# Optimization experiments

Hardware: AMD Instinct MI355X
Metric: run time of the kernel (lower is better)

Reference implementation:

```python
import jax, jax.numpy as jnp
import numpy as np

NUM_SLOTS = 24
EPS = 1e-5

def setup_inputs() -> dict:
    key = jax.random.key(0)
    k1, k2 = jax.random.split(key)
    x = jax.random.normal(k1, (4, 32, 200, 2048), dtype=jnp.float32)
    time = jax.random.randint(k2, (4, 2048), 0, NUM_SLOTS, dtype=jnp.int64)
    return {"x": x, "time": time}

def reference(x, time):
    # x: [b, c, n, t]; time: [b, t] int slot ids in [0, NUM_SLOTS)
    b, c, n, t = x.shape
    time = time[..., -t:]
    idx = time.reshape(b * t)

    # [b*t, n, c] layout matching x.permute(2,0,3,1).reshape(n, b*t, c) contraction
    xf = jnp.transpose(x, (0, 3, 2, 1)).reshape(b * t, n * c)

    # True segment-sum replaces the one-hot matmul; column L1-normalize == divide by slot count
    counts = jax.ops.segment_sum(jnp.ones((b * t,), x.dtype), idx, num_segments=NUM_SLOTS)
    denom = jnp.maximum(counts, 1e-12)[:, None]  # F.normalize eps-clamped norm

    sum_x = jax.ops.segment_sum(xf, idx, num_segments=NUM_SLOTS)            # [S, n*c]
    sum_x2 = jax.ops.segment_sum(xf * xf, idx, num_segments=NUM_SLOTS)      # [S, n*c]

    mean_slot = (sum_x / denom).reshape(NUM_SLOTS, n, c).mean(axis=1)       # [S, c]
    m2_slot = (sum_x2 / denom).reshape(NUM_SLOTS, n, c).mean(axis=1)        # [S, c]
    var_slot = m2_slot - mean_slot ** 2                                     # [S, c]

    # Embedding gather back per (b, t), broadcast over n
    sm = jnp.transpose(mean_slot[time], (0, 2, 1))[:, :, None, :]           # [b, c, 1, t]
    sv = jnp.transpose(var_slot[time], (0, 2, 1))[:, :, None, :]            # [b, c, 1, t]

    return (x - sm) / jnp.sqrt(sv + EPS)
```

## Files before the change

kernel.cpp:

```cpp
#include <hip/hip_runtime.h>
#include <math.h>

#define Bb 4
#define Cc 32
#define Nn 200
#define Tt 2048
#define Ss 24
#define EPSf 1e-5f
#define GRID2 512

typedef float f4 __attribute__((ext_vector_type(4)));
typedef int i4 __attribute__((ext_vector_type(4)));
typedef unsigned u4 __attribute__((ext_vector_type(4)));

__device__ __forceinline__ unsigned rne_bf16(float f) {
    unsigned u = __float_as_uint(f);
    return (u + 0x7FFFu + ((u >> 16) & 1u)) >> 16;
}
__device__ __forceinline__ unsigned pack2(float a, float b) {
    return rne_bf16(a) | (rne_bf16(b) << 16);
}
__device__ __forceinline__ float lo16(unsigned u) { return __uint_as_float(u << 16); }
__device__ __forceinline__ float hi16(unsigned u) { return __uint_as_float(u & 0xFFFF0000u); }


__global__ void k_zero(int* __restrict__ counter) { *counter = 0; }

#define ROWS16(M) M(0) M(1) M(2) M(3) M(4) M(5) M(6) M(7) \
                  M(8) M(9) M(10) M(11) M(12) M(13) M(14) M(15)

#define DROW(i) u4 xb##i;

#define LROW(i) { \
    f4 v0 = *(const f4*)(bp + (size_t)(i) * Tt); \
    f4 v1 = *(const f4*)(bp + (size_t)(i) * Tt + 4); \
    xb##i[0] = pack2(v0[0], v0[1]); \
    xb##i[1] = pack2(v0[2], v0[3]); \
    xb##i[2] = pack2(v1[0], v1[1]); \
    xb##i[3] = pack2(v1[2], v1[3]); \
    s0 += v0[0]; a0 += v0[0]*v0[0]; s1 += v0[1]; a1 += v0[1]*v0[1]; \
    s2 += v0[2]; a2 += v0[2]*v0[2]; s3 += v0[3]; a3 += v0[3]*v0[3]; \
    s4 += v1[0]; a4 += v1[0]*v1[0]; s5 += v1[1]; a5 += v1[1]*v1[1]; \
    s6 += v1[2]; a6 += v1[2]*v1[2]; s7 += v1[3]; a7 += v1[3]*v1[3]; }

#define SROW(i) { \
    f4 o0, o1; \
    o0[0] = fmaf(lo16(xb##i[0]), rr0, -mr0); \
    o0[1] = fmaf(hi16(xb##i[0]), rr1, -mr1); \
    o0[2] = fmaf(lo16(xb##i[1]), rr2, -mr2); \
    o0[3] = fmaf(hi16(xb##i[1]), rr3, -mr3); \
    o1[0] = fmaf(lo16(xb##i[2]), rr4, -mr4); \
    o1[1] = fmaf(hi16(xb##i[2]), rr5, -mr5); \
    o1[2] = fmaf(lo16(xb##i[3]), rr6, -mr6); \
    o1[3] = fmaf(hi16(xb##i[3]), rr7, -mr7); \
    __builtin_nontemporal_store(o0, (f4*)(op + (size_t)(i) * Tt)); \
    __builtin_nontemporal_store(o1, (f4*)(op + (size_t)(i) * Tt + 4)); }

__global__ __launch_bounds__(512) void k_fused(const float* __restrict__ x,
                                               const int* __restrict__ timei,
                                               float2* __restrict__ part,
                                               int* __restrict__ cntp,
                                               int* __restrict__ counter,
                                               float* __restrict__ out) {
    __shared__ unsigned ldsd[9 * 4 * 512];
    __shared__ float lsum[Ss], lsq[Ss];
    __shared__ int   lcnt[Ss];
    __shared__ float s_r[Ss], s_mr[Ss];

    const int tid = threadIdx.x;
    const int bx  = blockIdx.x;
    const int b   = bx >> 7;
    const int c   = (bx >> 2) & 31;
    const int qc  = bx & 3;
    const int rg  = tid >> 8;
    const int t0  = (tid & 255) * 8;

    if (tid < Ss) { lsum[tid] = 0.f; lsq[tid] = 0.f; lcnt[tid] = 0; }
    __syncthreads();

    const i4 sl0 = *(const i4*)(timei + b * Tt + t0);
    const i4 sl1 = *(const i4*)(timei + b * Tt + t0 + 4);

    const size_t plane = ((size_t)(b * Cc + c) * Nn + (size_t)qc * 50 + (size_t)rg * 25) * Tt + t0;
    const float* bp = x + plane;

    ROWS16(DROW)
    float s0=0,s1=0,s2=0,s3=0,s4=0,s5=0,s6=0,s7=0;
    float a0=0,a1=0,a2=0,a3=0,a4=0,a5=0,a6=0,a7=0;

    ROWS16(LROW)
    for (int r = 16; r < 25; ++r) {
        f4 v0 = *(const f4*)(bp + (size_t)r * Tt);
        f4 v1 = *(const f4*)(bp + (size_t)r * Tt + 4);
        const int base = (r - 16) * 4 * 512 + tid;
        ldsd[base]        = pack2(v0[0], v0[1]);
        ldsd[base + 512]  = pack2(v0[2], v0[3]);
        ldsd[base + 1024] = pack2(v1[0], v1[1]);
        ldsd[base + 1536] = pack2(v1[2], v1[3]);
        s0 += v0[0]; a0 += v0[0]*v0[0]; s1 += v0[1]; a1 += v0[1]*v0[1];
        s2 += v0[2]; a2 += v0[2]*v0[2]; s3 += v0[3]; a3 += v0[3]*v0[3];
        s4 += v1[0]; a4 += v1[0]*v1[0]; s5 += v1[1]; a5 += v1[1]*v1[1];
        s6 += v1[2]; a6 += v1[2]*v1[2]; s7 += v1[3]; a7 += v1[3]*v1[3];
    }

    atomicAdd(&lsum[sl0[0]], s0); atomicAdd(&lsq[sl0[0]], a0);
    atomicAdd(&lsum[sl0[1]], s1); atomicAdd(&lsq[sl0[1]], a1);
    atomicAdd(&lsum[sl0[2]], s2); atomicAdd(&lsq[sl0[2]], a2);
    atomicAdd(&lsum[sl0[3]], s3); atomicAdd(&lsq[sl0[3]], a3);
    atomicAdd(&lsum[sl1[0]], s4); atomicAdd(&lsq[sl1[0]], a4);
    atomicAdd(&lsum[sl1[1]], s5); atomicAdd(&lsq[sl1[1]], a5);
    atomicAdd(&lsum[sl1[2]], s6); atomicAdd(&lsq[sl1[2]], a6);
    atomicAdd(&lsum[sl1[3]], s7); atomicAdd(&lsq[sl1[3]], a7);
    if (c == 0 && qc == 0 && rg == 0) {
        atomicAdd(&lcnt[sl0[0]], 1); atomicAdd(&lcnt[sl0[1]], 1);
        atomicAdd(&lcnt[sl0[2]], 1); atomicAdd(&lcnt[sl0[3]], 1);
        atomicAdd(&lcnt[sl1[0]], 1); atomicAdd(&lcnt[sl1[1]], 1);
        atomicAdd(&lcnt[sl1[2]], 1); atomicAdd(&lcnt[sl1[3]], 1);
    }
    __syncthreads();

    if (tid < Ss) {
        part[(c * Ss + tid) * 16 + (b * 4 + qc)] = make_float2(lsum[tid], lsq[tid]);
        if (c == 0 && qc == 0) cntp[b * Ss + tid] = lcnt[tid];
    }
    __syncthreads();

    if (tid == 0) {
        __threadfence();
        __hip_atomic_fetch_add(counter, 1, __ATOMIC_ACQ_REL, __HIP_MEMORY_SCOPE_AGENT);
        while (__hip_atomic_load(counter, __ATOMIC_ACQUIRE, __HIP_MEMORY_SCOPE_AGENT) < GRID2)
            __builtin_amdgcn_s_sleep(2);
        __threadfence();
    }
    __syncthreads();

    if (tid < Ss) { lsum[tid] = 0.f; lsq[tid] = 0.f; }
    __syncthreads();
    if (tid < 192) {
        const int s = tid >> 3, j = tid & 7;
        float2 p0 = part[(c * Ss + s) * 16 + 2 * j];
        float2 p1 = part[(c * Ss + s) * 16 + 2 * j + 1];
        atomicAdd(&lsum[s], p0.x + p1.x);
        atomicAdd(&lsq[s],  p0.y + p1.y);
    }
    __syncthreads();
    if (tid < Ss) {
        int cnt = cntp[tid] + cntp[Ss + tid] + cntp[2 * Ss + tid] + cntp[3 * Ss + tid];
        float denom = fmaxf((float)cnt, 1e-12f) * (float)Nn;
        float m  = lsum[tid] / denom;
        float m2 = lsq[tid]  / denom;
        float rr = 1.0f / sqrtf(m2 - m * m + EPSf);
        s_r[tid]  = rr;
        s_mr[tid] = m * rr;
    }
    __syncthreads();

    const float rr0 = s_r[sl0[0]], mr0 = s_mr[sl0[0]];
    const float rr1 = s_r[sl0[1]], mr1 = s_mr[sl0[1]];
    const float rr2 = s_r[sl0[2]], mr2 = s_mr[sl0[2]];
    const float rr3 = s_r[sl0[3]], mr3 = s_mr[sl0[3]];
    const float rr4 = s_r[sl1[0]], mr4 = s_mr[sl1[0]];
    const float rr5 = s_r[sl1[1]], mr5 = s_mr[sl1[1]];
    const float rr6 = s_r[sl1[2]], mr6 = s_mr[sl1[2]];
    const float rr7 = s_r[sl1[3]], mr7 = s_mr[sl1[3]];

    float* op = out + plane;
    ROWS16(SROW)
    for (int r = 16; r < 25; ++r) {
        const int base = (r - 16) * 4 * 512 + tid;
        const unsigned w0 = ldsd[base];
        const unsigned w1 = ldsd[base + 512];
        const unsigned w2 = ldsd[base + 1024];
        const unsigned w3 = ldsd[base + 1536];
        f4 o0, o1;
        o0[0] = fmaf(lo16(w0), rr0, -mr0);
        o0[1] = fmaf(hi16(w0), rr1, -mr1);
        o0[2] = fmaf(lo16(w1), rr2, -mr2);
        o0[3] = fmaf(hi16(w1), rr3, -mr3);
        o1[0] = fmaf(lo16(w2), rr4, -mr4);
        o1[1] = fmaf(hi16(w2), rr5, -mr5);
        o1[2] = fmaf(lo16(w3), rr6, -mr6);
        o1[3] = fmaf(hi16(w3), rr7, -mr7);
        __builtin_nontemporal_store(o0, (f4*)(op + (size_t)r * Tt));
        __builtin_nontemporal_store(o1, (f4*)(op + (size_t)r * Tt + 4));
    }
}

__global__ __launch_bounds__(256) void k_stats(const float* __restrict__ x,
                                               const int* __restrict__ timei,
                                               float2* __restrict__ part,
                                               int* __restrict__ cntpart) {
    __shared__ float lsum[Ss], lsq[Ss];
    __shared__ int   lcnt[Ss];
    const int tid = threadIdx.x;
    const int bx  = blockIdx.x;
    const int tt = bx & 1;
    const int nc = (bx >> 1) & 7;
    const int bc = bx >> 4;
    const int b  = bc >> 5;
    const int c  = bc & 31;
    const bool do_hist = (c == 0 && nc == 0);

    if (tid < Ss) { lsum[tid] = 0.f; lsq[tid] = 0.f; lcnt[tid] = 0; }
    __syncthreads();

    const int t0 = tt * 1024 + tid * 4;
    const i4 sl = *(const i4*)(timei + b * Tt + t0);

    const size_t plane = ((size_t)(b * Cc + c) * Nn + (size_t)nc * 25) * Tt;
    const float* bp = x + plane + t0;

    float s0 = 0.f, s1 = 0.f, s2 = 0.f, s3 = 0.f;
    float q0 = 0.f, q1 = 0.f, q2 = 0.f, q3 = 0.f;
#pragma unroll 5
    for (int r = 0; r < 25; ++r) {
        f4 v = *(const f4*)(bp + (size_t)r * Tt);
        s0 += v[0]; q0 += v[0] * v[0];
        s1 += v[1]; q1 += v[1] * v[1];
        s2 += v[2]; q2 += v[2] * v[2];
        s3 += v[3]; q3 += v[3] * v[3];
    }

    atomicAdd(&lsum[sl[0]], s0); atomicAdd(&lsq[sl[0]], q0);
    atomicAdd(&lsum[sl[1]], s1); atomicAdd(&lsq[sl[1]], q1);
    atomicAdd(&lsum[sl[2]], s2); atomicAdd(&lsq[sl[2]], q2);
    atomicAdd(&lsum[sl[3]], s3); atomicAdd(&lsq[sl[3]], q3);
    if (do_hist) {
        atomicAdd(&lcnt[sl[0]], 1); atomicAdd(&lcnt[sl[1]], 1);
        atomicAdd(&lcnt[sl[2]], 1); atomicAdd(&lcnt[sl[3]], 1);
    }
    __syncthreads();

    const int chunk = (b * 2 + tt) * 8 + nc;
    if (tid < Ss) {
        part[(c * Ss + tid) * 64 + chunk] = make_float2(lsum[tid], lsq[tid]);
        if (do_hist) cntpart[(b * 2 + tt) * Ss + tid] = lcnt[tid];
    }
}

__global__ __launch_bounds__(256) void k_norm(const float* __restrict__ x,
                                              const int* __restrict__ timei,
                                              const float2* __restrict__ part,
                                              const int* __restrict__ cntpart,
                                              float* __restrict__ out) {
    __shared__ float lsum[Ss], lsq[Ss];
    __shared__ float s_mr[Ss], s_r[Ss];
    const int tid = threadIdx.x;
    const int bx  = blockIdx.x;
    const int b  = bx >> 7;
    const int c  = (bx >> 2) & 31;
    const int nc = bx & 3;

    if (tid < Ss) { lsum[tid] = 0.f; lsq[tid] = 0.f; }
    __syncthreads();
    if (tid < 192) {
        const int s = tid >> 3, j = tid & 7;
        const float2* pp = &part[(c * Ss + s) * 64 + j * 8];
        float ps = 0.f, pq = 0.f;
#pragma unroll
        for (int k = 0; k < 8; ++k) { ps += pp[k].x; pq += pp[k].y; }
        atomicAdd(&lsum[s], ps);
        atomicAdd(&lsq[s],  pq);
    }
    __syncthreads();
    if (tid < Ss) {
        int cnt = 0;
#pragma unroll
        for (int h = 0; h < 8; ++h) cnt += cntpart[h * Ss + tid];
        float denom = fmaxf((float)cnt, 1e-12f) * (float)Nn;
        float m  = lsum[tid] / denom;
        float m2 = lsq[tid]  / denom;
        float rr = 1.0f / sqrtf(m2 - m * m + EPSf);
        s_r[tid]  = rr;
        s_mr[tid] = m * rr;
    }
    __syncthreads();

    const int t0 = tid * 4;
    const i4 sl0 = *(const i4*)(timei + b * Tt + t0);
    const i4 sl1 = *(const i4*)(timei + b * Tt + t0 + 1024);
    const float rr0 = s_r[sl0[0]], mr0 = s_mr[sl0[0]];
    const float rr1 = s_r[sl0[1]], mr1 = s_mr[sl0[1]];
    const float rr2 = s_r[sl0[2]], mr2 = s_mr[sl0[2]];
    const float rr3 = s_r[sl0[3]], mr3 = s_mr[sl0[3]];
    const float rr4 = s_r[sl1[0]], mr4 = s_mr[sl1[0]];
    const float rr5 = s_r[sl1[1]], mr5 = s_mr[sl1[1]];
    const float rr6 = s_r[sl1[2]], mr6 = s_mr[sl1[2]];
    const float rr7 = s_r[sl1[3]], mr7 = s_mr[sl1[3]];

    const size_t plane = ((size_t)(b * Cc + c) * Nn + (size_t)nc * 50) * Tt;
    const float* xp = x + plane + t0;
    float* op = out + plane + t0;

#pragma unroll 5
    for (int r = 0; r < 50; ++r) {
        f4 v0 = *(const f4*)(xp + (size_t)r * Tt);
        f4 v1 = *(const f4*)(xp + (size_t)r * Tt + 1024);
        f4 o0, o1;
        o0[0] = fmaf(v0[0], rr0, -mr0);
        o0[1] = fmaf(v0[1], rr1, -mr1);
        o0[2] = fmaf(v0[2], rr2, -mr2);
        o0[3] = fmaf(v0[3], rr3, -mr3);
        o1[0] = fmaf(v1[0], rr4, -mr4);
        o1[1] = fmaf(v1[1], rr5, -mr5);
        o1[2] = fmaf(v1[2], rr6, -mr6);
        o1[3] = fmaf(v1[3], rr7, -mr7);
        __builtin_nontemporal_store(o0, (f4*)(op + (size_t)r * Tt));
        __builtin_nontemporal_store(o1, (f4*)(op + (size_t)r * Tt + 1024));
    }
}

extern "C" void kernel_launch(void* const* d_in, const int* in_sizes, int n_in,
                              void* d_out, int out_size, void* d_ws, size_t ws_size,
                              hipStream_t stream) {
    const float* x   = (const float*)d_in[0];
    const int* timei = (const int*)d_in[1];
    float* out = (float*)d_out;

    hipFuncAttributes fa;
    bool fused_ok = (hipFuncGetAttributes(&fa, (const void*)k_fused) == hipSuccess)
                    && fa.localSizeBytes == 0;
    if (fused_ok) {
        int occ = 0;
        fused_ok = (hipOccupancyMaxActiveBlocksPerMultiprocessor(&occ, k_fused, 512, 0)
                    == hipSuccess) && occ >= 2;
    }

    if (fused_ok) {
        float2* part = (float2*)d_ws;
        int* cntp    = (int*)((char*)d_ws + (size_t)Cc * Ss * 64 * sizeof(float2));
        int* counter = (int*)((char*)d_ws + (size_t)Cc * Ss * 64 * sizeof(float2)
                              + 128 * sizeof(int));
        k_zero<<<1, 1, 0, stream>>>(counter);
        k_fused<<<GRID2, 512, 0, stream>>>(x, timei, part, cntp, counter, out);
    } else {
        float2* part = (float2*)d_ws;
        int* cnt = (int*)((char*)d_ws + (size_t)Cc * Ss * 64 * sizeof(float2));
        k_stats<<<2048, 256, 0, stream>>>(x, timei, part, cnt);
        k_norm<<<512, 256, 0, stream>>>(x, timei, part, cnt, out);
    }
}
```

Measured before the change: 104.0 us.

## Split fused kernel caching: fewer register rows, smaller LDS, re-read tail rows

```diff
diff --git a/kernel.cpp b/kernel.cpp
--- a/kernel.cpp
+++ b/kernel.cpp
@@ -7,7 +7,7 @@
 #define Tt 2048
 #define Ss 24
 #define EPSf 1e-5f
-#define GRID2 512
+#define GRIDF 512
 
 typedef float f4 __attribute__((ext_vector_type(4)));
 typedef int i4 __attribute__((ext_vector_type(4)));
@@ -26,14 +26,13 @@
 
 __global__ void k_zero(int* __restrict__ counter) { *counter = 0; }
 
-#define ROWS16(M) M(0) M(1) M(2) M(3) M(4) M(5) M(6) M(7) \
-                  M(8) M(9) M(10) M(11) M(12) M(13) M(14) M(15)
+#define ROWS12(M) M(0) M(1) M(2) M(3) M(4) M(5) M(6) M(7) M(8) M(9) M(10) M(11)
 
 #define DROW(i) u4 xb##i;
 
 #define LROW(i) { \
     f4 v0 = *(const f4*)(bp + (size_t)(i) * Tt); \
-    f4 v1 = *(const f4*)(bp + (size_t)(i) * Tt + 4); \
+    f4 v1 = *(const f4*)(bp + (size_t)(i) * Tt + 1024); \
     xb##i[0] = pack2(v0[0], v0[1]); \
     xb##i[1] = pack2(v0[2], v0[3]); \
     xb##i[2] = pack2(v1[0], v1[1]); \
@@ -54,45 +53,46 @@
     o1[2] = fmaf(lo16(xb##i[3]), rr6, -mr6); \
     o1[3] = fmaf(hi16(xb##i[3]), rr7, -mr7); \
     __builtin_nontemporal_store(o0, (f4*)(op + (size_t)(i) * Tt)); \
-    __builtin_nontemporal_store(o1, (f4*)(op + (size_t)(i) * Tt + 4)); }
-
-__global__ __launch_bounds__(512) void k_fused(const float* __restrict__ x,
+    __builtin_nontemporal_store(o1, (f4*)(op + (size_t)(i) * Tt + 1024)); }
+
+__global__ __launch_bounds__(512) void k_fuse2(const float* __restrict__ x,
                                                const int* __restrict__ timei,
                                                float2* __restrict__ part,
                                                int* __restrict__ cntp,
                                                int* __restrict__ counter,
                                                float* __restrict__ out) {
-    __shared__ unsigned ldsd[9 * 4 * 512];
+    __shared__ unsigned ldsd[7 * 4 * 512];
     __shared__ float lsum[Ss], lsq[Ss];
     __shared__ int   lcnt[Ss];
     __shared__ float s_r[Ss], s_mr[Ss];
 
-    const int tid = threadIdx.x;
-    const int bx  = blockIdx.x;
-    const int b   = bx >> 7;
-    const int c   = (bx >> 2) & 31;
-    const int qc  = bx & 3;
-    const int rg  = tid >> 8;
-    const int t0  = (tid & 255) * 8;
+    const int tid  = threadIdx.x;
+    const int bx   = blockIdx.x;
+    const int b    = bx >> 7;
+    const int c    = (bx >> 2) & 31;
+    const int q    = bx & 3;
+    const int rg   = tid >> 8;
+    const int lane = tid & 255;
+    const int t0   = lane * 4;
 
     if (tid < Ss) { lsum[tid] = 0.f; lsq[tid] = 0.f; lcnt[tid] = 0; }
     __syncthreads();
 
     const i4 sl0 = *(const i4*)(timei + b * Tt + t0);
-    const i4 sl1 = *(const i4*)(timei + b * Tt + t0 + 4);
-
-    const size_t plane = ((size_t)(b * Cc + c) * Nn + (size_t)qc * 50 + (size_t)rg * 25) * Tt + t0;
+    const i4 sl1 = *(const i4*)(timei + b * Tt + t0 + 1024);
+
+    const size_t plane = ((size_t)(b * Cc + c) * Nn + (size_t)q * 50 + (size_t)rg * 25) * Tt + t0;
     const float* bp = x + plane;
 
-    ROWS16(DROW)
+    ROWS12(DROW)
     float s0=0,s1=0,s2=0,s3=0,s4=0,s5=0,s6=0,s7=0;
     float a0=0,a1=0,a2=0,a3=0,a4=0,a5=0,a6=0,a7=0;
 
-    ROWS16(LROW)
-    for (int r = 16; r < 25; ++r) {
+    ROWS12(LROW)
+    for (int r = 12; r < 19; ++r) {
         f4 v0 = *(const f4*)(bp + (size_t)r * Tt);
-        f4 v1 = *(const f4*)(bp + (size_t)r * Tt + 4);
-        const int base = (r - 16) * 4 * 512 + tid;
+        f4 v1 = *(const f4*)(bp + (size_t)r * Tt + 1024);
+        const int base = (r - 12) * 2048 + tid;
         ldsd[base]        = pack2(v0[0], v0[1]);
         ldsd[base + 512]  = pack2(v0[2], v0[3]);
         ldsd[base + 1024] = pack2(v1[0], v1[1]);
@@ -102,6 +102,14 @@
         s4 += v1[0]; a4 += v1[0]*v1[0]; s5 += v1[1]; a5 += v1[1]*v1[1];
         s6 += v1[2]; a6 += v1[2]*v1[2]; s7 += v1[3]; a7 += v1[3]*v1[3];
     }
+    for (int r = 19; r < 25; ++r) {
+        f4 v0 = *(const f4*)(bp + (size_t)r * Tt);
+        f4 v1 = *(const f4*)(bp + (size_t)r * Tt + 1024);
+        s0 += v0[0]; a0 += v0[0]*v0[0]; s1 += v0[1]; a1 += v0[1]*v0[1];
+        s2 += v0[2]; a2 += v0[2]*v0[2]; s3 += v0[3]; a3 += v0[3]*v0[3];
+        s4 += v1[0]; a4 += v1[0]*v1[0]; s5 += v1[1]; a5 += v1[1]*v1[1];
+        s6 += v1[2]; a6 += v1[2]*v1[2]; s7 += v1[3]; a7 += v1[3]*v1[3];
+    }
 
     atomicAdd(&lsum[sl0[0]], s0); atomicAdd(&lsq[sl0[0]], a0);
     atomicAdd(&lsum[sl0[1]], s1); atomicAdd(&lsq[sl0[1]], a1);
@@ -111,7 +119,7 @@
     atomicAdd(&lsum[sl1[1]], s5); atomicAdd(&lsq[sl1[1]], a5);
     atomicAdd(&lsum[sl1[2]], s6); atomicAdd(&lsq[sl1[2]], a6);
     atomicAdd(&lsum[sl1[3]], s7); atomicAdd(&lsq[sl1[3]], a7);
-    if (c == 0 && qc == 0 && rg == 0) {
+    if (c == 0 && q == 0 && rg == 0) {
         atomicAdd(&lcnt[sl0[0]], 1); atomicAdd(&lcnt[sl0[1]], 1);
         atomicAdd(&lcnt[sl0[2]], 1); atomicAdd(&lcnt[sl0[3]], 1);
         atomicAdd(&lcnt[sl1[0]], 1); atomicAdd(&lcnt[sl1[1]], 1);
@@ -120,15 +128,15 @@
     __syncthreads();
 
     if (tid < Ss) {
-        part[(c * Ss + tid) * 16 + (b * 4 + qc)] = make_float2(lsum[tid], lsq[tid]);
-        if (c == 0 && qc == 0) cntp[b * Ss + tid] = lcnt[tid];
+        part[(c * Ss + tid) * 16 + (b * 4 + q)] = make_float2(lsum[tid], lsq[tid]);
+        if (c == 0 && q == 0) cntp[b * Ss + tid] = lcnt[tid];
     }
     __syncthreads();
 
     if (tid == 0) {
         __threadfence();
         __hip_atomic_fetch_add(counter, 1, __ATOMIC_ACQ_REL, __HIP_MEMORY_SCOPE_AGENT);
-        while (__hip_atomic_load(counter, __ATOMIC_ACQUIRE, __HIP_MEMORY_SCOPE_AGENT) < GRID2)
+        while (__hip_atomic_load(counter, __ATOMIC_ACQUIRE, __HIP_MEMORY_SCOPE_AGENT) < GRIDF)
             __builtin_amdgcn_s_sleep(2);
         __threadfence();
     }
@@ -165,9 +173,9 @@
     const float rr7 = s_r[sl1[3]], mr7 = s_mr[sl1[3]];
 
     float* op = out + plane;
-    ROWS16(SROW)
-    for (int r = 16; r < 25; ++r) {
-        const int base = (r - 16) * 4 * 512 + tid;
+    ROWS12(SROW)
+    for (int r = 12; r < 19; ++r) {
+        const int base = (r - 12) * 2048 + tid;
         const unsigned w0 = ldsd[base];
         const unsigned w1 = ldsd[base + 512];
         const unsigned w2 = ldsd[base + 1024];
@@ -182,7 +190,22 @@
         o1[2] = fmaf(lo16(w3), rr6, -mr6);
         o1[3] = fmaf(hi16(w3), rr7, -mr7);
         __builtin_nontemporal_store(o0, (f4*)(op + (size_t)r * Tt));
-        __builtin_nontemporal_store(o1, (f4*)(op + (size_t)r * Tt + 4));
+        __builtin_nontemporal_store(o1, (f4*)(op + (size_t)r * Tt + 1024));
+    }
+    for (int r = 19; r < 25; ++r) {
+        f4 v0 = *(const f4*)(bp + (size_t)r * Tt);
+        f4 v1 = *(const f4*)(bp + (size_t)r * Tt + 1024);
+        f4 o0, o1;
+        o0[0] = fmaf(v0[0], rr0, -mr0);
+        o0[1] = fmaf(v0[1], rr1, -mr1);
+        o0[2] = fmaf(v0[2], rr2, -mr2);
+        o0[3] = fmaf(v0[3], rr3, -mr3);
+        o1[0] = fmaf(v1[0], rr4, -mr4);
+        o1[1] = fmaf(v1[1], rr5, -mr5);
+        o1[2] = fmaf(v1[2], rr6, -mr6);
+        o1[3] = fmaf(v1[3], rr7, -mr7);
+        __builtin_nontemporal_store(o0, (f4*)(op + (size_t)r * Tt));
+        __builtin_nontemporal_store(o1, (f4*)(op + (size_t)r * Tt + 1024));
     }
 }
 
@@ -318,21 +341,21 @@
     float* out = (float*)d_out;
 
     hipFuncAttributes fa;
-    bool fused_ok = (hipFuncGetAttributes(&fa, (const void*)k_fused) == hipSuccess)
+    bool fused_ok = (hipFuncGetAttributes(&fa, (const void*)k_fuse2) == hipSuccess)
                     && fa.localSizeBytes == 0;
     if (fused_ok) {
         int occ = 0;
-        fused_ok = (hipOccupancyMaxActiveBlocksPerMultiprocessor(&occ, k_fused, 512, 0)
+        fused_ok = (hipOccupancyMaxActiveBlocksPerMultiprocessor(&occ, k_fuse2, 512, 0)
                     == hipSuccess) && occ >= 2;
     }
 
     if (fused_ok) {
         float2* part = (float2*)d_ws;
-        int* cntp    = (int*)((char*)d_ws + (size_t)Cc * Ss * 64 * sizeof(float2));
-        int* counter = (int*)((char*)d_ws + (size_t)Cc * Ss * 64 * sizeof(float2)
+        int* cntp    = (int*)((char*)d_ws + (size_t)Cc * Ss * 16 * sizeof(float2));
+        int* counter = (int*)((char*)d_ws + (size_t)Cc * Ss * 16 * sizeof(float2)
                               + 128 * sizeof(int));
         k_zero<<<1, 1, 0, stream>>>(counter);
-        k_fused<<<GRID2, 512, 0, stream>>>(x, timei, part, cntp, counter, out);
+        k_fuse2<<<GRIDF, 512, 0, stream>>>(x, timei, part, cntp, counter, out);
     } else {
         float2* part = (float2*)d_ws;
         int* cnt = (int*)((char*)d_ws + (size_t)Cc * Ss * 64 * sizeof(float2));
```

Result: no change. 104.0 us (-0.0%).
